# Kernel tuning notes

Measured on AMD Instinct MI355X. Metric: run time of the kernel, lower is better.

## Reference

```python
import jax, jax.numpy as jnp
import numpy as np

EMB = 1024
DM = 64
NH = 16

def setup_inputs() -> dict:
    key = jax.random.key(0)
    ks = jax.random.split(key, 11)
    bs, slen = 2, 2048
    s = 1.0 / np.sqrt(EMB)
    inp = {
        'Q': jax.random.normal(ks[0], (bs, slen, EMB), jnp.float32),
        'K': jax.random.normal(ks[1], (bs, slen, EMB), jnp.float32),
        'V': jax.random.normal(ks[2], (bs, slen, EMB), jnp.float32),
        'Wq': jax.random.normal(ks[3], (EMB, DM * NH), jnp.float32) * s,
        'bq': jnp.zeros((DM * NH,), jnp.float32),
        'Wk': jax.random.normal(ks[4], (EMB, DM * NH), jnp.float32) * s,
        'bk': jnp.zeros((DM * NH,), jnp.float32),
        'Wv': jax.random.normal(ks[5], (EMB, DM * NH), jnp.float32) * s,
        'bv': jnp.zeros((DM * NH,), jnp.float32),
        'Wo': jax.random.normal(ks[6], (DM * NH, EMB), jnp.float32) * (1.0 / np.sqrt(DM * NH)),
        'bo': jnp.zeros((EMB,), jnp.float32),
    }
    return inp

def reference(Q, K, V, Wq, bq, Wk, bk, Wv, bv, Wo, bo):
    bs, q_len, _ = Q.shape
    kv_len = K.shape[1]
    scale = 1.0 / np.sqrt(DM)
    # project and split heads: (n, l, h, d)
    q = (scale * (Q @ Wq + bq)).reshape(bs, q_len, NH, DM)
    k = (K @ Wk + bk).reshape(bs, kv_len, NH, DM)
    v = (V @ Wv + bv).reshape(bs, kv_len, NH, DM)
    # scores (n, h, l, s) -- full S x S matrix, as in the original
    qk = jnp.einsum('nlhd,nshd->nhls', q, k)
    a = jax.nn.softmax(qk, axis=-1)  # dropout p=0 -> identity
    o = jnp.einsum('nhls,nshd->nlhd', a, v).reshape(bs, q_len, NH * DM)
    return o @ Wo + bo
```

## Files before the change

### kernel.cpp

```cpp
#include <hip/hip_runtime.h>
#include <cstdint>
#include <cstddef>

#define EMB  1024
#define DM   64
#define NH   16
#define SLEN 2048
#define BS   2

typedef _Float16 f16x8 __attribute__((ext_vector_type(8)));
typedef _Float16 f16x4 __attribute__((ext_vector_type(4)));
typedef __fp16   hf2   __attribute__((ext_vector_type(2)));
typedef __fp16   hf4   __attribute__((ext_vector_type(4)));
typedef float    f32x4 __attribute__((ext_vector_type(4)));

#define ASYNC_LD16(gp, lp)                                                        \
    __builtin_amdgcn_global_load_lds(                                             \
        (const __attribute__((address_space(1))) void*)(gp),                      \
        (__attribute__((address_space(3))) void*)(lp), 16, 0, 0)

__global__ __launch_bounds__(256)
void prep(const float* __restrict__ Q, const float* __restrict__ K,
          const float* __restrict__ V,
          const float* __restrict__ Wq, const float* __restrict__ Wk,
          const float* __restrict__ Wv, const float* __restrict__ Wo,
          _Float16* __restrict__ Qh, _Float16* __restrict__ Kh,
          _Float16* __restrict__ Vh,
          _Float16* __restrict__ WqT, _Float16* __restrict__ WkT,
          _Float16* __restrict__ WvT, _Float16* __restrict__ WoT)
{
    __shared__ float t[64][65];
    const int z = blockIdx.z;
    if (z < 3) {
        const float* in  = (z == 0) ? Q : (z == 1) ? K : V;
        _Float16*    out = (z == 0) ? Qh : (z == 1) ? Kh : Vh;
        size_t i = ((size_t)blockIdx.x * 256 + threadIdx.x) * 8;
        float4 a = *(const float4*)(in + i);
        float4 b = *(const float4*)(in + i + 4);
        f16x8 o;
        o[0] = (_Float16)a.x; o[1] = (_Float16)a.y; o[2] = (_Float16)a.z; o[3] = (_Float16)a.w;
        o[4] = (_Float16)b.x; o[5] = (_Float16)b.y; o[6] = (_Float16)b.z; o[7] = (_Float16)b.w;
        *(f16x8*)(out + i) = o;
        return;
    }
    if (blockIdx.x >= 256) return;
    const float* W;
    _Float16*    T;
    switch (z - 3) {
        case 0:  W = Wq; T = WqT; break;
        case 1:  W = Wk; T = WkT; break;
        case 2:  W = Wv; T = WvT; break;
        default: W = Wo; T = WoT; break;
    }
    const int tid = threadIdx.x;
    const int bn  = (blockIdx.x & 15) * 64;
    const int bk  = (blockIdx.x >> 4) * 64;

    #pragma unroll
    for (int p = 0; p < 4; ++p) {
        int row = p * 16 + (tid >> 4);
        int col = (tid & 15) * 4;
        float4 v = *(const float4*)(W + (size_t)(bk + row) * EMB + bn + col);
        t[row][col+0] = v.x; t[row][col+1] = v.y; t[row][col+2] = v.z; t[row][col+3] = v.w;
    }
    __syncthreads();
    #pragma unroll
    for (int p = 0; p < 4; ++p) {
        int nr = p * 16 + (tid >> 4);
        int kc = (tid & 15) * 4;
        f16x4 o;
        o[0] = (_Float16)t[kc+0][nr];
        o[1] = (_Float16)t[kc+1][nr];
        o[2] = (_Float16)t[kc+2][nr];
        o[3] = (_Float16)t[kc+3][nr];
        *(f16x4*)&T[(size_t)(bn + nr) * EMB + bk + kc] = o;
    }
}

__device__ __forceinline__
void gemm_core(const _Float16* __restrict__ A, const _Float16* __restrict__ Bt,
               const float* __restrict__ bias, float* __restrict__ Cf,
               _Float16* __restrict__ Ch, int M, int N, int K,
               float scale, int mode, int bx, int by)
{
    __shared__ __align__(16) _Float16 As[128 * 32];
    __shared__ __align__(16) _Float16 Bs[128 * 32];

    const int tid  = threadIdx.x;
    const int lane = tid & 63;
    const int wave = tid >> 6;
    const int c    = lane & 15;
    const int quad = lane >> 4;
    const int bm   = by * 128;
    const int bn   = bx * 128;
    const int wm   = (wave >> 1) * 64;
    const int wn   = (wave & 1) * 64;

    f32x4 acc[4][4];
    #pragma unroll
    for (int i = 0; i < 4; ++i)
        #pragma unroll
        for (int j = 0; j < 4; ++j)
            #pragma unroll
            for (int r = 0; r < 4; ++r) acc[i][j][r] = 0.f;

    const char* gA = (const char*)(A + (size_t)(bm + (tid >> 2)) * K) + (tid & 3) * 16;
    const char* gB = (const char*)(Bt + (size_t)(bn + (tid >> 2)) * K) + (tid & 3) * 16;
    char* lA = (char*)As + wave * 1024;
    char* lB = (char*)Bs + wave * 1024;
    const size_t rowskip = (size_t)64 * K * 2;

    for (int k0 = 0; k0 < K; k0 += 32) {
        __syncthreads();
        ASYNC_LD16(gA + (size_t)k0 * 2,           lA);
        ASYNC_LD16(gA + rowskip + (size_t)k0 * 2, lA + 4096);
        ASYNC_LD16(gB + (size_t)k0 * 2,           lB);
        ASYNC_LD16(gB + rowskip + (size_t)k0 * 2, lB + 4096);
        __syncthreads();

        f16x8 af[4], bf[4];
        #pragma unroll
        for (int i = 0; i < 4; ++i)
            af[i] = *(const f16x8*)&As[(wm + i * 16 + c) * 32 + quad * 8];
        #pragma unroll
        for (int j = 0; j < 4; ++j)
            bf[j] = *(const f16x8*)&Bs[(wn + j * 16 + c) * 32 + quad * 8];

        #pragma unroll
        for (int i = 0; i < 4; ++i)
            #pragma unroll
            for (int j = 0; j < 4; ++j)
                acc[i][j] = __builtin_amdgcn_mfma_f32_16x16x32_f16(af[i], bf[j], acc[i][j], 0, 0, 0);
    }

    float bcol[4];
    #pragma unroll
    for (int j = 0; j < 4; ++j) bcol[j] = bias[bn + wn + j * 16 + c];

    #pragma unroll
    for (int i = 0; i < 4; ++i) {
        int m0 = bm + wm + i * 16 + quad * 4;
        #pragma unroll
        for (int j = 0; j < 4; ++j) {
            int n = bn + wn + j * 16 + c;
            if (mode == 0) {
                #pragma unroll
                for (int r = 0; r < 4; ++r)
                    Cf[(size_t)(m0 + r) * N + n] = acc[i][j][r] + bcol[j];
            } else if (mode == 1) {
                int h = n >> 6, d = n & 63;
                #pragma unroll
                for (int r = 0; r < 4; ++r) {
                    int mm = m0 + r;
                    int b = mm >> 11, l = mm & (SLEN - 1);
                    Ch[(((size_t)(b * NH + h)) * SLEN + l) * DM + d] =
                        (_Float16)((acc[i][j][r] + bcol[j]) * scale);
                }
            } else {
                int h = n >> 6, d = n & 63;
                int b = m0 >> 11, l = m0 & (SLEN - 1);
                f16x4 o;
                #pragma unroll
                for (int r = 0; r < 4; ++r)
                    o[r] = (_Float16)(acc[i][j][r] + bcol[j]);
                *(f16x4*)&Ch[(((size_t)(b * NH + h)) * DM + d) * SLEN + l] = o;
            }
        }
    }
}

__global__ __launch_bounds__(256)
void gemm_qkv(const _Float16* __restrict__ Qh, const _Float16* __restrict__ Kh,
              const _Float16* __restrict__ Vh,
              const _Float16* __restrict__ WqT, const _Float16* __restrict__ WkT,
              const _Float16* __restrict__ WvT,
              const float* __restrict__ bq, const float* __restrict__ bk,
              const float* __restrict__ bv,
              _Float16* __restrict__ q_ws, _Float16* __restrict__ k_ws,
              _Float16* __restrict__ v_ws)
{
    const _Float16 *A, *Bt;
    const float* bias;
    _Float16* Ch;
    float scale;
    int mode;
    if (blockIdx.z == 0)      { A = Qh; Bt = WqT; bias = bq; Ch = q_ws; scale = 0.18033688f; mode = 1; }
    else if (blockIdx.z == 1) { A = Kh; Bt = WkT; bias = bk; Ch = k_ws; scale = 1.0f;        mode = 1; }
    else                      { A = Vh; Bt = WvT; bias = bv; Ch = v_ws; scale = 1.0f;        mode = 2; }
    gemm_core(A, Bt, bias, nullptr, Ch, BS * SLEN, NH * DM, EMB, scale, mode,
              blockIdx.x, blockIdx.y);
}

__global__ __launch_bounds__(256)
void gemm_out(const _Float16* __restrict__ Oh, const _Float16* __restrict__ WoT,
              const float* __restrict__ bo, float* __restrict__ out)
{
    gemm_core(Oh, WoT, bo, out, nullptr, BS * SLEN, EMB, NH * DM, 1.0f, 0,
              blockIdx.x, blockIdx.y);
}

__global__ __launch_bounds__(256)
void attn_mfma(const _Float16* __restrict__ qw, const _Float16* __restrict__ kw,
               const _Float16* __restrict__ vwT, _Float16* __restrict__ ow)
{
    __shared__ __align__(16) _Float16 Kt[2][64 * 64];
    __shared__ __align__(16) _Float16 Vt[2][64 * 64];

    const int tid  = threadIdx.x;
    const int lane = tid & 63;
    const int wave = tid >> 6;
    const int c    = lane & 15;
    const int quad = lane >> 4;
    const int bh   = blockIdx.y;
    const int b    = bh >> 4;
    const int h    = bh & 15;
    const int qbase = blockIdx.x * 128 + wave * 32;

    const _Float16* kb = kw  + (size_t)bh * SLEN * DM;
    const _Float16* vb = vwT + (size_t)bh * DM * SLEN;
    const _Float16* qb = qw  + (size_t)bh * SLEN * DM;

    f16x8 qf[2][2];
    #pragma unroll
    for (int t = 0; t < 2; ++t)
        #pragma unroll
        for (int ch = 0; ch < 2; ++ch)
            qf[t][ch] = *(const f16x8*)(qb + (size_t)(qbase + t*16 + c) * DM + ch*32 + quad*8);

    f32x4 oacc[2][4];
    f32x4 lacc[2];
    #pragma unroll
    for (int t = 0; t < 2; ++t) {
        #pragma unroll
        for (int dg = 0; dg < 4; ++dg)
            #pragma unroll
            for (int r = 0; r < 4; ++r) oacc[t][dg][r] = 0.f;
        #pragma unroll
        for (int r = 0; r < 4; ++r) lacc[t][r] = 0.f;
    }
    const f16x4 onesf = {(_Float16)1.f, (_Float16)1.f, (_Float16)1.f, (_Float16)1.f};
    const f32x4 zero4 = {0.f, 0.f, 0.f, 0.f};

    const int r0  = wave * 16 + (lane >> 3);
    const int lc0 = (((lane & 7) ^ (r0 & 7)) * 16);
    const char* gk = (const char*)kb + r0 * 128 + lc0;
    const char* gv = (const char*)vb + (size_t)r0 * 4096 + lc0;
    char* lK = (char*)&Kt[0][0] + wave * 2048;
    char* lV = (char*)&Vt[0][0] + wave * 2048;

    ASYNC_LD16(gk,         lK);
    ASYNC_LD16(gk + 1024,  lK + 1024);
    ASYNC_LD16(gv,         lV);
    ASYNC_LD16(gv + 32768, lV + 1024);
    gk += 8192; gv += 128;
    __syncthreads();

    auto tile = [&](int cur) {
        {
            char* pk = (char*)&Kt[cur ^ 1][0] + wave * 2048;
            char* pv = (char*)&Vt[cur ^ 1][0] + wave * 2048;
            ASYNC_LD16(gk,         pk);
            ASYNC_LD16(gk + 1024,  pk + 1024);
            ASYNC_LD16(gv,         pv);
            ASYNC_LD16(gv + 32768, pv + 1024);
            gk += 8192; gv += 128;
        }

        f16x8 kf[4][2];
        #pragma unroll
        for (int g = 0; g < 4; ++g)
            #pragma unroll
            for (int ch = 0; ch < 2; ++ch)
                kf[g][ch] = *(const f16x8*)
                    &Kt[cur][(g*16 + c) * 64 + (((ch*4 + quad) ^ (c & 7)) * 8)];

        f32x4 s[2][4];
        #pragma unroll
        for (int t = 0; t < 2; ++t)
            #pragma unroll
            for (int g = 0; g < 4; ++g) {
                s[t][g] = __builtin_amdgcn_mfma_f32_16x16x32_f16(kf[g][0], qf[t][0], zero4,   0, 0, 0);
                s[t][g] = __builtin_amdgcn_mfma_f32_16x16x32_f16(kf[g][1], qf[t][1], s[t][g], 0, 0, 0);
            }

        f16x4 pf[2][4];
        #pragma unroll
        for (int t = 0; t < 2; ++t)
            #pragma unroll
            for (int g = 0; g < 4; ++g) {
                float p0 = __builtin_amdgcn_exp2f(s[t][g][0]);
                float p1 = __builtin_amdgcn_exp2f(s[t][g][1]);
                float p2 = __builtin_amdgcn_exp2f(s[t][g][2]);
                float p3 = __builtin_amdgcn_exp2f(s[t][g][3]);
                hf2 lo = __builtin_amdgcn_cvt_pkrtz(p0, p1);
                hf2 hi = __builtin_amdgcn_cvt_pkrtz(p2, p3);
                hf4 pv = __builtin_shufflevector(lo, hi, 0, 1, 2, 3);
                pf[t][g] = __builtin_bit_cast(f16x4, pv);
            }

        #pragma unroll
        for (int g = 0; g < 4; ++g) {
            lacc[0] = __builtin_amdgcn_mfma_f32_16x16x16f16(pf[0][g], onesf, lacc[0], 0, 0, 0);
            lacc[1] = __builtin_amdgcn_mfma_f32_16x16x16f16(pf[1][g], onesf, lacc[1], 0, 0, 0);
        }

        #pragma unroll
        for (int dg = 0; dg < 4; ++dg) {
            f16x4 vf[4];
            #pragma unroll
            for (int g = 0; g < 4; ++g)
                vf[g] = *(const f16x4*)
                    &Vt[cur][(dg*16 + c) * 64 +
                             (((2*g + (quad >> 1)) ^ (c & 7)) * 8) + (quad & 1) * 4];
            #pragma unroll
            for (int g = 0; g < 4; ++g)
                #pragma unroll
                for (int t = 0; t < 2; ++t)
                    oacc[t][dg] = __builtin_amdgcn_mfma_f32_16x16x16f16(pf[t][g], vf[g], oacc[t][dg], 0, 0, 0);
        }
        __syncthreads();
    };

    for (int it = 0; it < SLEN / 64; it += 2) {
        tile(0);
        tile(1);
    }

    #pragma unroll
    for (int t = 0; t < 2; ++t) {
        #pragma unroll
        for (int r = 0; r < 4; ++r) {
            float linv = 1.0f / lacc[t][r];
            int row = qbase + t*16 + quad*4 + r;
            #pragma unroll
            for (int dg = 0; dg < 4; ++dg)
                ow[((size_t)b * SLEN + row) * EMB + h * DM + dg*16 + c] =
                    (_Float16)(oacc[t][dg][r] * linv);
        }
    }
}

extern "C" void kernel_launch(void* const* d_in, const int* in_sizes, int n_in,
                              void* d_out, int out_size, void* d_ws, size_t ws_size,
                              hipStream_t stream)
{
    const float* Q  = (const float*)d_in[0];
    const float* K  = (const float*)d_in[1];
    const float* V  = (const float*)d_in[2];
    const float* Wq = (const float*)d_in[3];
    const float* bq = (const float*)d_in[4];
    const float* Wk = (const float*)d_in[5];
    const float* bk = (const float*)d_in[6];
    const float* Wv = (const float*)d_in[7];
    const float* bv = (const float*)d_in[8];
    const float* Wo = (const float*)d_in[9];
    const float* bo = (const float*)d_in[10];
    float* out = (float*)d_out;

    const size_t MN = (size_t)BS * SLEN * NH * DM;
    const size_t WW = (size_t)EMB * NH * DM;

    _Float16* base = (_Float16*)d_ws;
    _Float16* Qh   = base;
    _Float16* Kh   = Qh  + MN;
    _Float16* Vh   = Kh  + MN;
    _Float16* WqT  = Vh  + MN;
    _Float16* WkT  = WqT + WW;
    _Float16* WvT  = WkT + WW;
    _Float16* WoT  = WvT + WW;
    _Float16* q_ws = WoT + WW;
    _Float16* k_ws = q_ws + MN;
    _Float16* v_ws = k_ws + MN;
    _Float16* o_ws = v_ws + MN;

    dim3 blk(256);

    prep<<<dim3(2048, 1, 7), blk, 0, stream>>>(Q, K, V, Wq, Wk, Wv, Wo,
                                               Qh, Kh, Vh, WqT, WkT, WvT, WoT);

    gemm_qkv<<<dim3(8, 32, 3), blk, 0, stream>>>(Qh, Kh, Vh, WqT, WkT, WvT,
                                                 bq, bk, bv, q_ws, k_ws, v_ws);

    attn_mfma<<<dim3(SLEN / 128, BS * NH), blk, 0, stream>>>(q_ws, k_ws, v_ws, o_ws);

    gemm_out<<<dim3(8, 32, 1), blk, 0, stream>>>(o_ws, WoT, bo, out);
}
```

Measured before the change: 236.9 us.

## Split attention over two KV halves with merge kernel; halve GEMM M-tile

The attention kernel is split along the key/value sequence into two halves via a new grid z dimension. Each half writes unnormalized fp32 partial outputs and row sums into workspace that aliases the now-dead converted inputs, and a new merge kernel sums and normalizes them into the fp16 output. Separately, the QKV and output GEMMs use a 64x128 tile with an occupancy hint of 5 blocks per SM, doubling the block count. The aim is better CU fill on a 512-block attention grid and the GEMMs. The cost is extra fp32 partial traffic, an additional launch, and less operand reuse per GEMM block. The merge is only valid if the partials share a common softmax reference rather than separate running maxima.

New measurement: 250.9 us. +5.9%, slower.

```diff
diff --git a/kernel.cpp b/kernel.cpp
--- a/kernel.cpp
+++ b/kernel.cpp
@@ -78,12 +78,12 @@
 }
 
 __device__ __forceinline__
-void gemm_core(const _Float16* __restrict__ A, const _Float16* __restrict__ Bt,
-               const float* __restrict__ bias, float* __restrict__ Cf,
-               _Float16* __restrict__ Ch, int M, int N, int K,
-               float scale, int mode, int bx, int by)
-{
-    __shared__ __align__(16) _Float16 As[128 * 32];
+void gemm_core64(const _Float16* __restrict__ A, const _Float16* __restrict__ Bt,
+                 const float* __restrict__ bias, float* __restrict__ Cf,
+                 _Float16* __restrict__ Ch, int M, int N, int K,
+                 float scale, int mode, int bx, int by)
+{
+    __shared__ __align__(16) _Float16 As[64 * 32];
     __shared__ __align__(16) _Float16 Bs[128 * 32];
 
     const int tid  = threadIdx.x;
@@ -91,14 +91,14 @@
     const int wave = tid >> 6;
     const int c    = lane & 15;
     const int quad = lane >> 4;
-    const int bm   = by * 128;
+    const int bm   = by * 64;
     const int bn   = bx * 128;
-    const int wm   = (wave >> 1) * 64;
+    const int wm   = (wave >> 1) * 32;
     const int wn   = (wave & 1) * 64;
 
-    f32x4 acc[4][4];
-    #pragma unroll
-    for (int i = 0; i < 4; ++i)
+    f32x4 acc[2][4];
+    #pragma unroll
+    for (int i = 0; i < 2; ++i)
         #pragma unroll
         for (int j = 0; j < 4; ++j)
             #pragma unroll
@@ -108,26 +108,25 @@
     const char* gB = (const char*)(Bt + (size_t)(bn + (tid >> 2)) * K) + (tid & 3) * 16;
     char* lA = (char*)As + wave * 1024;
     char* lB = (char*)Bs + wave * 1024;
-    const size_t rowskip = (size_t)64 * K * 2;
+    const size_t rowskipB = (size_t)64 * K * 2;
 
     for (int k0 = 0; k0 < K; k0 += 32) {
         __syncthreads();
-        ASYNC_LD16(gA + (size_t)k0 * 2,           lA);
-        ASYNC_LD16(gA + rowskip + (size_t)k0 * 2, lA + 4096);
-        ASYNC_LD16(gB + (size_t)k0 * 2,           lB);
-        ASYNC_LD16(gB + rowskip + (size_t)k0 * 2, lB + 4096);
+        ASYNC_LD16(gA + (size_t)k0 * 2,            lA);
+        ASYNC_LD16(gB + (size_t)k0 * 2,            lB);
+        ASYNC_LD16(gB + rowskipB + (size_t)k0 * 2, lB + 4096);
         __syncthreads();
 
-        f16x8 af[4], bf[4];
-        #pragma unroll
-        for (int i = 0; i < 4; ++i)
+        f16x8 af[2], bf[4];
+        #pragma unroll
+        for (int i = 0; i < 2; ++i)
             af[i] = *(const f16x8*)&As[(wm + i * 16 + c) * 32 + quad * 8];
         #pragma unroll
         for (int j = 0; j < 4; ++j)
             bf[j] = *(const f16x8*)&Bs[(wn + j * 16 + c) * 32 + quad * 8];
 
         #pragma unroll
-        for (int i = 0; i < 4; ++i)
+        for (int i = 0; i < 2; ++i)
             #pragma unroll
             for (int j = 0; j < 4; ++j)
                 acc[i][j] = __builtin_amdgcn_mfma_f32_16x16x32_f16(af[i], bf[j], acc[i][j], 0, 0, 0);
@@ -138,7 +137,7 @@
     for (int j = 0; j < 4; ++j) bcol[j] = bias[bn + wn + j * 16 + c];
 
     #pragma unroll
-    for (int i = 0; i < 4; ++i) {
+    for (int i = 0; i < 2; ++i) {
         int m0 = bm + wm + i * 16 + quad * 4;
         #pragma unroll
         for (int j = 0; j < 4; ++j) {
@@ -169,7 +168,7 @@
     }
 }
 
-__global__ __launch_bounds__(256)
+__global__ __launch_bounds__(256, 5)
 void gemm_qkv(const _Float16* __restrict__ Qh, const _Float16* __restrict__ Kh,
               const _Float16* __restrict__ Vh,
               const _Float16* __restrict__ WqT, const _Float16* __restrict__ WkT,
@@ -187,21 +186,22 @@
     if (blockIdx.z == 0)      { A = Qh; Bt = WqT; bias = bq; Ch = q_ws; scale = 0.18033688f; mode = 1; }
     else if (blockIdx.z == 1) { A = Kh; Bt = WkT; bias = bk; Ch = k_ws; scale = 1.0f;        mode = 1; }
     else                      { A = Vh; Bt = WvT; bias = bv; Ch = v_ws; scale = 1.0f;        mode = 2; }
-    gemm_core(A, Bt, bias, nullptr, Ch, BS * SLEN, NH * DM, EMB, scale, mode,
-              blockIdx.x, blockIdx.y);
-}
-
-__global__ __launch_bounds__(256)
+    gemm_core64(A, Bt, bias, nullptr, Ch, BS * SLEN, NH * DM, EMB, scale, mode,
+                blockIdx.x, blockIdx.y);
+}
+
+__global__ __launch_bounds__(256, 5)
 void gemm_out(const _Float16* __restrict__ Oh, const _Float16* __restrict__ WoT,
               const float* __restrict__ bo, float* __restrict__ out)
 {
-    gemm_core(Oh, WoT, bo, out, nullptr, BS * SLEN, EMB, NH * DM, 1.0f, 0,
-              blockIdx.x, blockIdx.y);
+    gemm_core64(Oh, WoT, bo, out, nullptr, BS * SLEN, EMB, NH * DM, 1.0f, 0,
+                blockIdx.x, blockIdx.y);
 }
 
 __global__ __launch_bounds__(256)
 void attn_mfma(const _Float16* __restrict__ qw, const _Float16* __restrict__ kw,
-               const _Float16* __restrict__ vwT, _Float16* __restrict__ ow)
+               const _Float16* __restrict__ vwT,
+               float* __restrict__ Opart, float* __restrict__ lpart)
 {
     __shared__ __align__(16) _Float16 Kt[2][64 * 64];
     __shared__ __align__(16) _Float16 Vt[2][64 * 64];
@@ -212,12 +212,11 @@
     const int c    = lane & 15;
     const int quad = lane >> 4;
     const int bh   = blockIdx.y;
-    const int b    = bh >> 4;
-    const int h    = bh & 15;
+    const int kz   = blockIdx.z;
     const int qbase = blockIdx.x * 128 + wave * 32;
 
-    const _Float16* kb = kw  + (size_t)bh * SLEN * DM;
-    const _Float16* vb = vwT + (size_t)bh * DM * SLEN;
+    const _Float16* kb = kw  + (size_t)bh * SLEN * DM + (size_t)kz * 1024 * DM;
+    const _Float16* vb = vwT + (size_t)bh * DM * SLEN + (size_t)kz * 1024;
     const _Float16* qb = qw  + (size_t)bh * SLEN * DM;
 
     f16x8 qf[2][2];
@@ -321,23 +320,48 @@
         __syncthreads();
     };
 
-    for (int it = 0; it < SLEN / 64; it += 2) {
+    for (int it = 0; it < 1024 / 64; it += 2) {
         tile(0);
         tile(1);
     }
 
+    const size_t pbase = ((size_t)kz * 32 + bh) * SLEN;
     #pragma unroll
     for (int t = 0; t < 2; ++t) {
+        if (c == 0) {
+            #pragma unroll
+            for (int r = 0; r < 4; ++r)
+                lpart[pbase + qbase + t*16 + quad*4 + r] = lacc[t][r];
+        }
         #pragma unroll
         for (int r = 0; r < 4; ++r) {
-            float linv = 1.0f / lacc[t][r];
             int row = qbase + t*16 + quad*4 + r;
             #pragma unroll
             for (int dg = 0; dg < 4; ++dg)
-                ow[((size_t)b * SLEN + row) * EMB + h * DM + dg*16 + c] =
-                    (_Float16)(oacc[t][dg][r] * linv);
-        }
-    }
+                Opart[(pbase + row) * 64 + dg*16 + c] = oacc[t][dg][r];
+        }
+    }
+}
+
+__global__ __launch_bounds__(256)
+void attn_merge(const float* __restrict__ Opart, const float* __restrict__ lpart,
+                _Float16* __restrict__ ow)
+{
+    size_t idx = ((size_t)blockIdx.x * 256 + threadIdx.x) * 4;
+    int bh  = (int)(idx >> 17);
+    int rem = (int)(idx & 131071);
+    int row = rem >> 6, d = rem & 63;
+    float4 o0 = *(const float4*)(Opart + idx);
+    float4 o1 = *(const float4*)(Opart + (1u << 22) + idx);
+    float l = lpart[(size_t)bh * SLEN + row] + lpart[65536 + (size_t)bh * SLEN + row];
+    float inv = 1.0f / l;
+    int b = bh >> 4, h = bh & 15;
+    f16x4 o;
+    o[0] = (_Float16)((o0.x + o1.x) * inv);
+    o[1] = (_Float16)((o0.y + o1.y) * inv);
+    o[2] = (_Float16)((o0.z + o1.z) * inv);
+    o[3] = (_Float16)((o0.w + o1.w) * inv);
+    *(f16x4*)&ow[((size_t)b * SLEN + row) * EMB + h * DM + d] = o;
 }
 
 extern "C" void kernel_launch(void* const* d_in, const int* in_sizes, int n_in,
@@ -367,21 +391,26 @@
     _Float16* WqT  = Vh  + MN;
     _Float16* WkT  = WqT + WW;
     _Float16* WvT  = WkT + WW;
-    _Float16* WoT  = WvT + WW;
+    _Float16* WoT  = base + 16 * 1024 * 1024;
     _Float16* q_ws = WoT + WW;
     _Float16* k_ws = q_ws + MN;
     _Float16* v_ws = k_ws + MN;
     _Float16* o_ws = v_ws + MN;
+    float*    lpart = (float*)(o_ws + MN);
+    float*    Opart = (float*)d_ws;
 
     dim3 blk(256);
 
     prep<<<dim3(2048, 1, 7), blk, 0, stream>>>(Q, K, V, Wq, Wk, Wv, Wo,
                                                Qh, Kh, Vh, WqT, WkT, WvT, WoT);
 
-    gemm_qkv<<<dim3(8, 32, 3), blk, 0, stream>>>(Qh, Kh, Vh, WqT, WkT, WvT,
+    gemm_qkv<<<dim3(8, 64, 3), blk, 0, stream>>>(Qh, Kh, Vh, WqT, WkT, WvT,
                                                  bq, bk, bv, q_ws, k_ws, v_ws);
 
-    attn_mfma<<<dim3(SLEN / 128, BS * NH), blk, 0, stream>>>(q_ws, k_ws, v_ws, o_ws);
-
-    gemm_out<<<dim3(8, 32, 1), blk, 0, stream>>>(o_ws, WoT, bo, out);
-}
+    attn_mfma<<<dim3(SLEN / 128, BS * NH, 2), blk, 0, stream>>>(q_ws, k_ws, v_ws,
+                                                                Opart, lpart);
+
+    attn_merge<<<dim3(4096), blk, 0, stream>>>(Opart, lpart, o_ws);
+
+    gemm_out<<<dim3(8, 64, 1), blk, 0, stream>>>(o_ws, WoT, bo, out);
+}
```
